# Kernel optimization log

Hardware: AMD Instinct MI355X
Metric: run time of the kernel (lower is better)

Reference implementation:

```python
import jax, jax.numpy as jnp
import numpy as np

N, IN_DIM, L, K, D = 131072, 128, 16, 8, 50
ENC_H, DEC_H, HEAD_H, DF = 64, 16, 64, 1.0


def setup_inputs() -> dict:
    key = jax.random.key(0)
    ks = jax.random.split(key, 20)
    s = lambda k, shape, fan: jax.random.normal(k, shape, jnp.float32) * (1.0 / np.sqrt(fan))
    return {
        "x": jax.random.normal(ks[0], (N, IN_DIM), jnp.float32),
        # encoder: in -> 64 -> 64 -> L
        "We1": s(ks[1], (IN_DIM, ENC_H), IN_DIM), "be1": jnp.zeros((ENC_H,), jnp.float32),
        "We2": s(ks[2], (ENC_H, ENC_H), ENC_H),   "be2": jnp.zeros((ENC_H,), jnp.float32),
        "We3": s(ks[3], (ENC_H, L), ENC_H),       "be3": jnp.zeros((L,), jnp.float32),
        # decoder: L -> 16 -> in
        "Wd1": s(ks[4], (L, DEC_H), L),           "bd1": jnp.zeros((DEC_H,), jnp.float32),
        "Wd2": s(ks[5], (DEC_H, IN_DIM), DEC_H),  "bd2": jnp.zeros((IN_DIM,), jnp.float32),
        # K per-cluster survival heads: (L+in) -> 64 -> num_durations
        "Wh1": s(ks[6], (K, L + IN_DIM, HEAD_H), L + IN_DIM), "bh1": jnp.zeros((K, HEAD_H), jnp.float32),
        "Wh2": s(ks[7], (K, HEAD_H, D), HEAD_H),              "bh2": jnp.zeros((K, D), jnp.float32),
        # cluster centers buffer
        "centers": jax.random.normal(ks[8], (K, L), jnp.float32) * 0.05,
    }


def _student_t_sim(z, centers, df):
    # z: [N, L], centers: [K, L] -> q: [N, K]
    dist2 = jnp.sum((z[:, None, :] - centers[None, :, :]) ** 2, axis=-1)
    logits = -0.5 * (df + 1.0) * jnp.log1p(dist2 / df)
    return jax.nn.softmax(logits, axis=1)


def reference(x, We1, be1, We2, be2, We3, be3, Wd1, bd1, Wd2, bd2,
              Wh1, bh1, Wh2, bh2, centers):
    relu = jax.nn.relu
    # encoder (eval mode: dropout off, non-variational)
    e = relu(x @ We1 + be1)
    e = relu(e @ We2 + be2)
    z = e @ We3 + be3                      # [N, L]
    q = _student_t_sim(z, centers, DF)     # [N, K]
    h = jnp.concatenate([z, x], axis=1)    # [N, L+in]
    # cluster-argmax routing to per-cluster heads: compute all K, select winner
    cluster_idx = jnp.argmax(q, axis=1)    # [N]
    h1 = relu(jnp.einsum("nf,kfh->nkh", h, Wh1) + bh1[None])   # [N, K, H]
    lg = jnp.einsum("nkh,khd->nkd", h1, Wh2) + bh2[None]       # [N, K, D]
    surv_logits = jnp.take_along_axis(lg, cluster_idx[:, None, None], axis=1)[:, 0]  # [N, D]
    # decoder + reconstruction loss per sample
    d = relu(z @ Wd1 + bd1)
    x_hat = d @ Wd2 + bd2                  # [N, in]
    rec_ps = jnp.mean((x_hat - x) ** 2, axis=1)
    kld = jnp.zeros((x.shape[0],), x.dtype)
    return z, q, surv_logits, x_hat, rec_ps, kld
```

## Files before the change

kernel.cpp:

```cpp
#include <hip/hip_runtime.h>

#define NS 131072
#define KC 8
typedef unsigned long long u64;

#define LD4(P) (*reinterpret_cast<const float4*>(&sm[(P)]))
#define ST4(P) (*reinterpret_cast<float4*>(&sm[(P)]))
#define GL4(P) (*reinterpret_cast<const float4*>(&(P)))

#define FMA4(ACCR, AV, B) do { \
  ACCR[0]=fmaf((AV),(B).x,ACCR[0]); ACCR[1]=fmaf((AV),(B).y,ACCR[1]); \
  ACCR[2]=fmaf((AV),(B).z,ACCR[2]); ACCR[3]=fmaf((AV),(B).w,ACCR[3]); } while(0)

#define K4(ACC, ABASE, ASTR, AK, BBASE, BSTR, JOFF, BK) do { \
  const float4 b0=LD4((BBASE)+((BK)*4+0)*(BSTR)+(JOFF)); \
  const float4 b1=LD4((BBASE)+((BK)*4+1)*(BSTR)+(JOFF)); \
  const float4 b2=LD4((BBASE)+((BK)*4+2)*(BSTR)+(JOFF)); \
  const float4 b3=LD4((BBASE)+((BK)*4+3)*(BSTR)+(JOFF)); \
  _Pragma("unroll") \
  for (int m_ = 0; m_ < 8; ++m_) { \
    const float4 av = LD4((ABASE)+(st+8*m_)*(ASTR)+(AK)*4); \
    FMA4(ACC[m_], av.x, b0); FMA4(ACC[m_], av.y, b1); \
    FMA4(ACC[m_], av.z, b2); FMA4(ACC[m_], av.w, b3); } \
} while(0)

#define INIT84(ACC, BPTR, OFF) do { \
  const float4 u_ = *reinterpret_cast<const float4*>(&(BPTR)[(OFF)]); \
  _Pragma("unroll") for (int m_=0;m_<8;++m_){ \
    ACC[m_][0]=u_.x; ACC[m_][1]=u_.y; ACC[m_][2]=u_.z; ACC[m_][3]=u_.w; } } while(0)

#define RELU84(ACC) do { _Pragma("unroll") for (int m_=0;m_<8;++m_) \
  { _Pragma("unroll") for (int j_=0;j_<4;++j_) ACC[m_][j_]=fmaxf(ACC[m_][j_],0.f); } } while(0)

#define WRITE_E(ACC) do { _Pragma("unroll") for (int m_=0;m_<8;++m_){ \
  ST4(EA + (st+8*m_)*68 + job) = \
    make_float4(ACC[m_][0],ACC[m_][1],ACC[m_][2],ACC[m_][3]); } } while(0)

#define STAGE_XB(B) do { \
  ST4((B) + xr0*20 + xcc)     = rx0; \
  ST4((B) + xr0*20 + xcc + 4) = rx1; } while(0)
#define STAGE_WB(B) do { \
  ST4((B) + wr*68 + wcc)     = rw0; \
  ST4((B) + wr*68 + wcc + 4) = rw1; } while(0)

#define XA   0
#define XB   1280
#define WA   2560
#define WB_  3648
#define EA   4736
#define ZD   4736
#define SMW  9088

__global__ __launch_bounds__(128, 2) void k_enc(
    const float* __restrict__ x,
    const float* __restrict__ We1, const float* __restrict__ be1,
    const float* __restrict__ We2, const float* __restrict__ be2,
    const float* __restrict__ We3, const float* __restrict__ be3,
    const float* __restrict__ Wd1, const float* __restrict__ bd1,
    const float* __restrict__ Wd2, const float* __restrict__ bd2,
    const float* __restrict__ centers,
    float* __restrict__ out_z, float* __restrict__ out_q,
    float* __restrict__ xhat, float* __restrict__ rec, float* __restrict__ kld,
    int* __restrict__ cidx, int* __restrict__ counts)
{
    __shared__ float sm[SMW];
    const int t  = threadIdx.x;
    const int ot = t & 15, st = t >> 4;
    const int job = ot * 4;
    const int s0 = blockIdx.x * 64;
    const int xr0 = t >> 1, xcc = (t & 1) * 8;
    const int wr  = t >> 3, wcc = (t & 7) * 8;

    {
        float acc1[8][4];
        INIT84(acc1, be1, job);
        ST4(XA + xr0*20 + xcc)     = GL4(x[(size_t)(s0+xr0)*128 + xcc]);
        ST4(XA + xr0*20 + xcc + 4) = GL4(x[(size_t)(s0+xr0)*128 + xcc + 4]);
        ST4(WA + wr*68 + wcc)      = GL4(We1[(size_t)wr*64 + wcc]);
        ST4(WA + wr*68 + wcc + 4)  = GL4(We1[(size_t)wr*64 + wcc + 4]);
        float4 rx0 = GL4(x[(size_t)(s0+xr0)*128 + 16 + xcc]);
        float4 rx1 = GL4(x[(size_t)(s0+xr0)*128 + 16 + xcc + 4]);
        float4 rw0 = GL4(We1[(size_t)(16 + wr)*64 + wcc]);
        float4 rw1 = GL4(We1[(size_t)(16 + wr)*64 + wcc + 4]);
        __syncthreads();
        #pragma unroll 1
        for (int c = 0; c < 8; ++c) {
            const int XC = (c & 1) ? XB : XA, WC = (c & 1) ? WB_ : WA;
            const int XN = (c & 1) ? XA : XB, WN = (c & 1) ? WA : WB_;
            #pragma unroll
            for (int kc = 0; kc < 4; ++kc) K4(acc1, XC, 20, kc, WC, 68, job, kc);
            if (c < 7) { STAGE_XB(XN); STAGE_WB(WN); }
            if (c < 6) {
                rx0 = GL4(x[(size_t)(s0+xr0)*128 + (c+2)*16 + xcc]);
                rx1 = GL4(x[(size_t)(s0+xr0)*128 + (c+2)*16 + xcc + 4]);
                rw0 = GL4(We1[(size_t)((c+2)*16 + wr)*64 + wcc]);
                rw1 = GL4(We1[(size_t)((c+2)*16 + wr)*64 + wcc + 4]);
            }
            if (c < 7) __syncthreads();
        }
        RELU84(acc1);
        WRITE_E(acc1);
    }

    {
        float acc2[8][4];
        INIT84(acc2, be2, job);
        ST4(WA + wr*68 + wcc)     = GL4(We2[(size_t)wr*64 + wcc]);
        ST4(WA + wr*68 + wcc + 4) = GL4(We2[(size_t)wr*64 + wcc + 4]);
        float4 rw0 = GL4(We2[(size_t)(16 + wr)*64 + wcc]);
        float4 rw1 = GL4(We2[(size_t)(16 + wr)*64 + wcc + 4]);
        __syncthreads();
        #pragma unroll 1
        for (int c = 0; c < 4; ++c) {
            const int WC = (c & 1) ? WB_ : WA, WN = (c & 1) ? WA : WB_;
            #pragma unroll
            for (int kc = 0; kc < 4; ++kc) K4(acc2, EA, 68, c*4 + kc, WC, 68, job, kc);
            if (c < 3) STAGE_WB(WN);
            if (c < 2) {
                rw0 = GL4(We2[(size_t)((c+2)*16 + wr)*64 + wcc]);
                rw1 = GL4(We2[(size_t)((c+2)*16 + wr)*64 + wcc + 4]);
            }
            if (c < 3) __syncthreads();
        }
        RELU84(acc2);
        WRITE_E(acc2);
    }

    ST4(XA + xr0*16 + xcc)     = GL4(We3[(size_t)xr0*16 + xcc]);
    ST4(XA + xr0*16 + xcc + 4) = GL4(We3[(size_t)xr0*16 + xcc + 4]);
    if (t < 32) {
        ST4(XB + (t>>1)*16 + (t&1)*8)     = GL4(Wd1[(t>>1)*16 + (t&1)*8]);
        ST4(XB + (t>>1)*16 + (t&1)*8 + 4) = GL4(Wd1[(t>>1)*16 + (t&1)*8 + 4]);
    }
    __syncthreads();

    float zac[8];
    {   const float b3v = be3[ot];
        #pragma unroll
        for (int m = 0; m < 8; ++m) zac[m] = b3v; }
    #pragma unroll 2
    for (int kc = 0; kc < 16; ++kc) {
        const float w0 = sm[XA + (kc*4+0)*16 + ot];
        const float w1 = sm[XA + (kc*4+1)*16 + ot];
        const float w2 = sm[XA + (kc*4+2)*16 + ot];
        const float w3 = sm[XA + (kc*4+3)*16 + ot];
        #pragma unroll
        for (int m = 0; m < 8; ++m) {
            const float4 av = LD4(EA + (st + 8*m)*68 + kc*4);
            float s = zac[m];
            s = fmaf(av.x, w0, s); s = fmaf(av.y, w1, s);
            s = fmaf(av.z, w2, s); s = fmaf(av.w, w3, s);
            zac[m] = s;
        }
    }
    #pragma unroll
    for (int m = 0; m < 8; ++m)
        out_z[(size_t)(s0 + st + 8*m)*16 + ot] = zac[m];
    __syncthreads();

    #pragma unroll
    for (int m = 0; m < 8; ++m) sm[ZD + (st + 8*m)*20 + ot] = zac[m];
    ST4(WA  + wr*68 + wcc)     = GL4(Wd2[(size_t)wr*128 + wcc]);
    ST4(WA  + wr*68 + wcc + 4) = GL4(Wd2[(size_t)wr*128 + wcc + 4]);
    ST4(WB_ + wr*68 + wcc)     = GL4(Wd2[(size_t)wr*128 + 64 + wcc]);
    ST4(WB_ + wr*68 + wcc + 4) = GL4(Wd2[(size_t)wr*128 + 64 + wcc + 4]);
    __syncthreads();

    if (t < 64) {
        const float4 z0 = LD4(ZD + t*20 + 0), z1 = LD4(ZD + t*20 + 4);
        const float4 z2 = LD4(ZD + t*20 + 8), z3 = LD4(ZD + t*20 + 12);
        const float zz[16] = {z0.x,z0.y,z0.z,z0.w, z1.x,z1.y,z1.z,z1.w,
                              z2.x,z2.y,z2.z,z2.w, z3.x,z3.y,z3.z,z3.w};
        float d2[KC];
        #pragma unroll
        for (int k = 0; k < KC; ++k) {
            float acc = 0.f;
            #pragma unroll
            for (int l = 0; l < 16; ++l) {
                const float dl = zz[l] - centers[k*16 + l];
                acc = fmaf(dl, dl, acc);
            }
            d2[k] = acc;
        }
        float lgt[KC], ex[KC];
        float mm = -1e30f;
        #pragma unroll
        for (int k = 0; k < KC; ++k) { lgt[k] = -log1pf(d2[k]); mm = fmaxf(mm, lgt[k]); }
        float ssum = 0.f;
        #pragma unroll
        for (int k = 0; k < KC; ++k) { ex[k] = expf(lgt[k] - mm); ssum += ex[k]; }
        const float inv = 1.f / ssum;
        float4* oq = reinterpret_cast<float4*>(&out_q[(size_t)(s0 + t)*8]);
        oq[0] = make_float4(ex[0]*inv, ex[1]*inv, ex[2]*inv, ex[3]*inv);
        oq[1] = make_float4(ex[4]*inv, ex[5]*inv, ex[6]*inv, ex[7]*inv);
        int ci = 0; float best = d2[0];
        #pragma unroll
        for (int k = 1; k < KC; ++k) if (d2[k] < best) { best = d2[k]; ci = k; }
        cidx[s0 + t] = ci;
        #pragma unroll
        for (int k = 0; k < KC; ++k) {
            const u64 mk = __ballot(ci == k);
            if (t == 0 && mk) atomicAdd(&counts[k], (int)__popcll(mk));
        }
        kld[s0 + t] = 0.f;
    }

    {
        float w[16];
        #pragma unroll
        for (int k = 0; k < 16; ++k) w[k] = sm[XB + k*16 + ot];
        const float bb = bd1[ot];
        float dac[8];
        #pragma unroll
        for (int m = 0; m < 8; ++m) {
            const int r = st + 8*m;
            float s = bb;
            #pragma unroll
            for (int kc = 0; kc < 4; ++kc) {
                const float4 av = LD4(ZD + r*20 + kc*4);
                s = fmaf(av.x, w[kc*4+0], s); s = fmaf(av.y, w[kc*4+1], s);
                s = fmaf(av.z, w[kc*4+2], s); s = fmaf(av.w, w[kc*4+3], s);
            }
            dac[m] = fmaxf(s, 0.f);
        }
        __syncthreads();
        #pragma unroll
        for (int m = 0; m < 8; ++m) sm[ZD + (st + 8*m)*20 + ot] = dac[m];
    }

    float rp[8] = {0.f,0.f,0.f,0.f,0.f,0.f,0.f,0.f};
    #pragma unroll
    for (int h = 0; h < 2; ++h) {
        const int WH = h ? WB_ : WA;
        float accx[8][4];
        INIT84(accx, bd2, h*64 + job);
        #pragma unroll
        for (int kc = 0; kc < 4; ++kc) K4(accx, ZD, 20, kc, WH, 68, job, kc);
        #pragma unroll
        for (int m = 0; m < 8; ++m) {
            const int r = st + 8*m;
            const float4 xa = GL4(x[(size_t)(s0+r)*128 + h*64 + job]);
            float df;
            df=accx[m][0]-xa.x; rp[m]=fmaf(df,df,rp[m]);
            df=accx[m][1]-xa.y; rp[m]=fmaf(df,df,rp[m]);
            df=accx[m][2]-xa.z; rp[m]=fmaf(df,df,rp[m]);
            df=accx[m][3]-xa.w; rp[m]=fmaf(df,df,rp[m]);
            *reinterpret_cast<float4*>(&xhat[(size_t)(s0+r)*128 + h*64 + job]) =
                make_float4(accx[m][0],accx[m][1],accx[m][2],accx[m][3]);
        }
    }
    #pragma unroll
    for (int m = 0; m < 8; ++m) {
        float v = rp[m];
        v += __shfl_xor(v, 1); v += __shfl_xor(v, 2);
        v += __shfl_xor(v, 4); v += __shfl_xor(v, 8);
        if (ot == 0) rec[s0 + st + 8*m] = v * (1.f/128.f);
    }
}

__global__ void k_scan(const int* __restrict__ counts,
                       int* __restrict__ bases, int* __restrict__ cursors)
{
    if (threadIdx.x == 0) {
        int acc = 0;
        for (int k = 0; k < KC; ++k) { bases[k] = acc; cursors[k] = acc; acc += counts[k]; }
    }
}

__global__ __launch_bounds__(256) void k_scatter(
    const int* __restrict__ cidx, int* __restrict__ cursors, int* __restrict__ seg)
{
    const int s = blockIdx.x * 256 + threadIdx.x;
    const int lane = threadIdx.x & 63;
    const int ci = cidx[s];
    #pragma unroll
    for (int k = 0; k < KC; ++k) {
        const u64 mk = __ballot(ci == k);
        if (ci == k) {
            const int leader = __ffsll(mk) - 1;
            int base = 0;
            if (lane == leader) base = atomicAdd(&cursors[k], (int)__popcll(mk));
            base = __shfl(base, leader, 64);
            seg[base + (int)__popcll(mk & (((u64)1 << lane) - 1))] = s;
        }
    }
}

__global__ __launch_bounds__(128, 2) void k_heads(
    const float* __restrict__ x, const float* __restrict__ zread,
    const float* __restrict__ Wh1, const float* __restrict__ bh1,
    const float* __restrict__ Wh2, const float* __restrict__ bh2,
    const int* __restrict__ counts, const int* __restrict__ bases,
    const int* __restrict__ seg,
    float* __restrict__ surv)
{
    __shared__ float sm[SMW];
    __shared__ int idxs[64];
    const int t  = threadIdx.x;
    const int ot = t & 15, st = t >> 4;
    const int job = ot * 4;
    const int xr0 = t >> 1, xcc = (t & 1) * 8;
    const int wr  = t >> 3, wcc = (t & 7) * 8;

    int kk = -1, chunk = 0, pref = 0;
    #pragma unroll
    for (int q = 0; q < KC; ++q) {
        const int ck = (counts[q] + 63) >> 6;
        if (kk < 0) {
            if ((int)blockIdx.x < pref + ck) { kk = q; chunk = (int)blockIdx.x - pref; }
            pref += ck;
        }
    }
    if (kk < 0) return;
    kk    = __builtin_amdgcn_readfirstlane(kk);
    chunk = __builtin_amdgcn_readfirstlane(chunk);
    const int cnt  = __builtin_amdgcn_readfirstlane(counts[kk]);
    const int base = __builtin_amdgcn_readfirstlane(bases[kk]);

    if (t < 64) {
        const int i = chunk*64 + t;
        idxs[t] = seg[base + ((i < cnt) ? i : (cnt - 1))];
    }
    __syncthreads();
    const int irow = idxs[xr0];

    {
        float acc1[8][4];
        INIT84(acc1, bh1, (size_t)kk*64 + job);
        ST4(XA + xr0*20 + xcc)     = GL4(zread[(size_t)irow*16 + xcc]);
        ST4(XA + xr0*20 + xcc + 4) = GL4(zread[(size_t)irow*16 + xcc + 4]);
        ST4(WA + wr*68 + wcc)      = GL4(Wh1[((size_t)kk*144 + wr)*64 + wcc]);
        ST4(WA + wr*68 + wcc + 4)  = GL4(Wh1[((size_t)kk*144 + wr)*64 + wcc + 4]);
        float4 rx0 = GL4(x[(size_t)irow*128 + xcc]);
        float4 rx1 = GL4(x[(size_t)irow*128 + xcc + 4]);
        float4 rw0 = GL4(Wh1[((size_t)kk*144 + 16 + wr)*64 + wcc]);
        float4 rw1 = GL4(Wh1[((size_t)kk*144 + 16 + wr)*64 + wcc + 4]);
        __syncthreads();
        #pragma unroll 1
        for (int c = 0; c < 9; ++c) {
            const int XC = (c & 1) ? XB : XA, WC = (c & 1) ? WB_ : WA;
            const int XN = (c & 1) ? XA : XB, WN = (c & 1) ? WA : WB_;
            #pragma unroll
            for (int kc = 0; kc < 4; ++kc) K4(acc1, XC, 20, kc, WC, 68, job, kc);
            if (c < 8) { STAGE_XB(XN); STAGE_WB(WN); }
            if (c < 7) {
                rx0 = GL4(x[(size_t)irow*128 + (c+1)*16 + xcc]);
                rx1 = GL4(x[(size_t)irow*128 + (c+1)*16 + xcc + 4]);
                rw0 = GL4(Wh1[((size_t)kk*144 + (c+2)*16 + wr)*64 + wcc]);
                rw1 = GL4(Wh1[((size_t)kk*144 + (c+2)*16 + wr)*64 + wcc + 4]);
            }
            if (c < 8) __syncthreads();
        }
        RELU84(acc1);
        WRITE_E(acc1);
    }
    __syncthreads();

    float acc2[8][4];
    {
        #pragma unroll
        for (int m = 0; m < 8; ++m) {
            acc2[m][0] = (job+0 < 50) ? bh2[(size_t)kk*50 + job+0] : 0.f;
            acc2[m][1] = (job+1 < 50) ? bh2[(size_t)kk*50 + job+1] : 0.f;
            acc2[m][2] = (job+2 < 50) ? bh2[(size_t)kk*50 + job+2] : 0.f;
            acc2[m][3] = (job+3 < 50) ? bh2[(size_t)kk*50 + job+3] : 0.f;
        }
    }
    #define LDWH2(RV0, RV1, CROW) do { \
        const size_t wrow_ = ((size_t)kk*64 + (CROW) + wr)*50; \
        RV0.x = (wcc+0 < 50) ? Wh2[wrow_ + wcc+0] : 0.f; \
        RV0.y = (wcc+1 < 50) ? Wh2[wrow_ + wcc+1] : 0.f; \
        RV0.z = (wcc+2 < 50) ? Wh2[wrow_ + wcc+2] : 0.f; \
        RV0.w = (wcc+3 < 50) ? Wh2[wrow_ + wcc+3] : 0.f; \
        RV1.x = (wcc+4 < 50) ? Wh2[wrow_ + wcc+4] : 0.f; \
        RV1.y = (wcc+5 < 50) ? Wh2[wrow_ + wcc+5] : 0.f; \
        RV1.z = (wcc+6 < 50) ? Wh2[wrow_ + wcc+6] : 0.f; \
        RV1.w = (wcc+7 < 50) ? Wh2[wrow_ + wcc+7] : 0.f; } while(0)
    {
        float4 rw0, rw1;
        LDWH2(rw0, rw1, 0);
        STAGE_WB(WA);
        LDWH2(rw0, rw1, 16);
        __syncthreads();
        #pragma unroll 1
        for (int c = 0; c < 4; ++c) {
            const int WC = (c & 1) ? WB_ : WA, WN = (c & 1) ? WA : WB_;
            #pragma unroll
            for (int kc = 0; kc < 4; ++kc) K4(acc2, EA, 68, c*4 + kc, WC, 68, job, kc);
            if (c < 3) STAGE_WB(WN);
            if (c < 2) LDWH2(rw0, rw1, (c+2)*16);
            if (c < 3) __syncthreads();
        }
    }
    #undef LDWH2

    #pragma unroll
    for (int m = 0; m < 8; ++m) {
        const int r = st + 8*m;
        if (chunk*64 + r < cnt) {
            float* so = &surv[(size_t)idxs[r]*50 + job];
            if (ot < 12) {
                *reinterpret_cast<float2*>(&so[0]) = make_float2(acc2[m][0], acc2[m][1]);
                *reinterpret_cast<float2*>(&so[2]) = make_float2(acc2[m][2], acc2[m][3]);
            } else if (ot == 12) {
                *reinterpret_cast<float2*>(&so[0]) = make_float2(acc2[m][0], acc2[m][1]);
            }
        }
    }
}

extern "C" void kernel_launch(void* const* d_in, const int* in_sizes, int n_in,
                              void* d_out, int out_size, void* d_ws, size_t ws_size,
                              hipStream_t stream)
{
    const float* x   = (const float*)d_in[0];
    const float* We1 = (const float*)d_in[1];
    const float* be1 = (const float*)d_in[2];
    const float* We2 = (const float*)d_in[3];
    const float* be2 = (const float*)d_in[4];
    const float* We3 = (const float*)d_in[5];
    const float* be3 = (const float*)d_in[6];
    const float* Wd1 = (const float*)d_in[7];
    const float* bd1 = (const float*)d_in[8];
    const float* Wd2 = (const float*)d_in[9];
    const float* bd2 = (const float*)d_in[10];
    const float* Wh1 = (const float*)d_in[11];
    const float* bh1 = (const float*)d_in[12];
    const float* Wh2 = (const float*)d_in[13];
    const float* bh2 = (const float*)d_in[14];
    const float* cen = (const float*)d_in[15];
    float* out = (float*)d_out;

    float* out_z  = out;
    float* out_q  = out + (size_t)NS * 16;
    float* out_sv = out + (size_t)NS * 24;
    float* out_xh = out + (size_t)NS * 74;
    float* out_rc = out + (size_t)NS * 202;
    float* out_kl = out + (size_t)NS * 203;

    int* cidx    = (int*)d_ws;
    int* counts  = cidx + NS;
    int* bases   = counts + KC;
    int* cursors = bases + KC;
    int* seg     = cursors + KC;

    hipMemsetAsync(counts, 0, KC * sizeof(int), stream);

    k_enc<<<dim3(NS / 64), dim3(128), 0, stream>>>(
        x, We1, be1, We2, be2, We3, be3, Wd1, bd1, Wd2, bd2, cen,
        out_z, out_q, out_xh, out_rc, out_kl, cidx, counts);

    k_scan<<<dim3(1), dim3(64), 0, stream>>>(counts, bases, cursors);

    k_scatter<<<dim3(NS / 256), dim3(256), 0, stream>>>(cidx, cursors, seg);

    k_heads<<<dim3(NS / 64 + KC), dim3(128), 0, stream>>>(
        x, out_z, Wh1, bh1, Wh2, bh2, counts, bases, seg, out_sv);
}
```

Measured before the change: 485.2 us.

## Stage GEMM tiles via async global-to-LDS loads in encoder and heads

Replaces register-staged double buffering of x, We1, We2, Wd2 and Wh1 tiles with __builtin_amdgcn_global_load_lds direct copies into unpadded LDS buffers. This removes the register round-trip and the VGPR pressure of holding prefetched tiles, and shrinks shared memory. In exchange, rows become unpadded with stride 16/64, which may add LDS bank conflicts. Correctness now depends on the barrier placement to order the async writes against reads.

```diff
diff --git a/kernel.cpp b/kernel.cpp
--- a/kernel.cpp
+++ b/kernel.cpp
@@ -8,15 +8,19 @@
 #define ST4(P) (*reinterpret_cast<float4*>(&sm[(P)]))
 #define GL4(P) (*reinterpret_cast<const float4*>(&(P)))
 
+#define ASYNC16(GP, LP) \
+  __builtin_amdgcn_global_load_lds((const __attribute__((address_space(1))) void*)(GP), \
+                                   (__attribute__((address_space(3))) void*)(LP), 16, 0, 0)
+
 #define FMA4(ACCR, AV, B) do { \
   ACCR[0]=fmaf((AV),(B).x,ACCR[0]); ACCR[1]=fmaf((AV),(B).y,ACCR[1]); \
   ACCR[2]=fmaf((AV),(B).z,ACCR[2]); ACCR[3]=fmaf((AV),(B).w,ACCR[3]); } while(0)
 
-#define K4(ACC, ABASE, ASTR, AK, BBASE, BSTR, JOFF, BK) do { \
-  const float4 b0=LD4((BBASE)+((BK)*4+0)*(BSTR)+(JOFF)); \
-  const float4 b1=LD4((BBASE)+((BK)*4+1)*(BSTR)+(JOFF)); \
-  const float4 b2=LD4((BBASE)+((BK)*4+2)*(BSTR)+(JOFF)); \
-  const float4 b3=LD4((BBASE)+((BK)*4+3)*(BSTR)+(JOFF)); \
+#define K4S(ACC, ABASE, ASTR, AK, BBASE, JOFF, BK) do { \
+  const float4 b0=LD4((BBASE)+((BK)*4+0)*64+(JOFF)); \
+  const float4 b1=LD4((BBASE)+((BK)*4+1)*64+(JOFF)); \
+  const float4 b2=LD4((BBASE)+((BK)*4+2)*64+(JOFF)); \
+  const float4 b3=LD4((BBASE)+((BK)*4+3)*64+(JOFF)); \
   _Pragma("unroll") \
   for (int m_ = 0; m_ < 8; ++m_) { \
     const float4 av = LD4((ABASE)+(st+8*m_)*(ASTR)+(AK)*4); \
@@ -36,20 +40,34 @@
   ST4(EA + (st+8*m_)*68 + job) = \
     make_float4(ACC[m_][0],ACC[m_][1],ACC[m_][2],ACC[m_][3]); } } while(0)
 
-#define STAGE_XB(B) do { \
-  ST4((B) + xr0*20 + xcc)     = rx0; \
-  ST4((B) + xr0*20 + xcc + 4) = rx1; } while(0)
-#define STAGE_WB(B) do { \
-  ST4((B) + wr*68 + wcc)     = rw0; \
-  ST4((B) + wr*68 + wcc + 4) = rw1; } while(0)
-
 #define XA   0
-#define XB   1280
-#define WA   2560
-#define WB_  3648
-#define EA   4736
-#define ZD   4736
-#define SMW  9088
+#define XB   1024
+#define WA   2048
+#define WB_  3072
+#define EA   4096
+#define ZD   4096
+#define SMW  8448
+
+#define ISSUE_XENC(BX, COL0) do { \
+  { const int r_ = (wv*2+0)*16 + (l>>2); \
+    ASYNC16(&x[(size_t)(s0+r_)*128 + (COL0) + (l&3)*4], &sm[(BX) + (wv*2+0)*256]); } \
+  { const int r_ = (wv*2+1)*16 + (l>>2); \
+    ASYNC16(&x[(size_t)(s0+r_)*128 + (COL0) + (l&3)*4], &sm[(BX) + (wv*2+1)*256]); } \
+} while(0)
+
+#define ISSUE_W16(BW, WPTR, ROW0) do { \
+  { const int r_ = (wv*2+0)*4 + (l>>4); \
+    ASYNC16(&(WPTR)[(size_t)((ROW0)+r_)*64 + (l&15)*4], &sm[(BW) + (wv*2+0)*256]); } \
+  { const int r_ = (wv*2+1)*4 + (l>>4); \
+    ASYNC16(&(WPTR)[(size_t)((ROW0)+r_)*64 + (l&15)*4], &sm[(BW) + (wv*2+1)*256]); } \
+} while(0)
+
+#define ISSUE_WD2(BW, HOFF) do { \
+  { const int r_ = (wv*2+0)*4 + (l>>4); \
+    ASYNC16(&Wd2[(size_t)r_*128 + (HOFF) + (l&15)*4], &sm[(BW) + (wv*2+0)*256]); } \
+  { const int r_ = (wv*2+1)*4 + (l>>4); \
+    ASYNC16(&Wd2[(size_t)r_*128 + (HOFF) + (l&15)*4], &sm[(BW) + (wv*2+1)*256]); } \
+} while(0)
 
 __global__ __launch_bounds__(128, 2) void k_enc(
     const float* __restrict__ x,
@@ -68,71 +86,49 @@
     const int ot = t & 15, st = t >> 4;
     const int job = ot * 4;
     const int s0 = blockIdx.x * 64;
-    const int xr0 = t >> 1, xcc = (t & 1) * 8;
-    const int wr  = t >> 3, wcc = (t & 7) * 8;
-
-    {
-        float acc1[8][4];
-        INIT84(acc1, be1, job);
-        ST4(XA + xr0*20 + xcc)     = GL4(x[(size_t)(s0+xr0)*128 + xcc]);
-        ST4(XA + xr0*20 + xcc + 4) = GL4(x[(size_t)(s0+xr0)*128 + xcc + 4]);
-        ST4(WA + wr*68 + wcc)      = GL4(We1[(size_t)wr*64 + wcc]);
-        ST4(WA + wr*68 + wcc + 4)  = GL4(We1[(size_t)wr*64 + wcc + 4]);
-        float4 rx0 = GL4(x[(size_t)(s0+xr0)*128 + 16 + xcc]);
-        float4 rx1 = GL4(x[(size_t)(s0+xr0)*128 + 16 + xcc + 4]);
-        float4 rw0 = GL4(We1[(size_t)(16 + wr)*64 + wcc]);
-        float4 rw1 = GL4(We1[(size_t)(16 + wr)*64 + wcc + 4]);
+    const int wv = t >> 6, l = t & 63;
+
+    float acc1[8][4];
+    INIT84(acc1, be1, job);
+    ISSUE_XENC(XA, 0);  ISSUE_W16(WA, We1, 0);
+    ISSUE_XENC(XB, 16); ISSUE_W16(WB_, We1, 16);
+    __syncthreads();
+    #pragma unroll 1
+    for (int c = 0; c < 8; ++c) {
+        const int XC = (c & 1) ? XB : XA, WC = (c & 1) ? WB_ : WA;
+        #pragma unroll
+        for (int kc = 0; kc < 4; ++kc) K4S(acc1, XC, 16, kc, WC, job, kc);
         __syncthreads();
-        #pragma unroll 1
-        for (int c = 0; c < 8; ++c) {
-            const int XC = (c & 1) ? XB : XA, WC = (c & 1) ? WB_ : WA;
-            const int XN = (c & 1) ? XA : XB, WN = (c & 1) ? WA : WB_;
-            #pragma unroll
-            for (int kc = 0; kc < 4; ++kc) K4(acc1, XC, 20, kc, WC, 68, job, kc);
-            if (c < 7) { STAGE_XB(XN); STAGE_WB(WN); }
-            if (c < 6) {
-                rx0 = GL4(x[(size_t)(s0+xr0)*128 + (c+2)*16 + xcc]);
-                rx1 = GL4(x[(size_t)(s0+xr0)*128 + (c+2)*16 + xcc + 4]);
-                rw0 = GL4(We1[(size_t)((c+2)*16 + wr)*64 + wcc]);
-                rw1 = GL4(We1[(size_t)((c+2)*16 + wr)*64 + wcc + 4]);
-            }
-            if (c < 7) __syncthreads();
-        }
-        RELU84(acc1);
-        WRITE_E(acc1);
-    }
+        if (c < 6) { ISSUE_XENC(XC, (c+2)*16); ISSUE_W16(WC, We1, (c+2)*16); }
+    }
+    RELU84(acc1);
+    WRITE_E(acc1);
 
     {
         float acc2[8][4];
         INIT84(acc2, be2, job);
-        ST4(WA + wr*68 + wcc)     = GL4(We2[(size_t)wr*64 + wcc]);
-        ST4(WA + wr*68 + wcc + 4) = GL4(We2[(size_t)wr*64 + wcc + 4]);
-        float4 rw0 = GL4(We2[(size_t)(16 + wr)*64 + wcc]);
-        float4 rw1 = GL4(We2[(size_t)(16 + wr)*64 + wcc + 4]);
+        ISSUE_W16(WA, We2, 0); ISSUE_W16(WB_, We2, 16);
         __syncthreads();
         #pragma unroll 1
         for (int c = 0; c < 4; ++c) {
-            const int WC = (c & 1) ? WB_ : WA, WN = (c & 1) ? WA : WB_;
+            const int WC = (c & 1) ? WB_ : WA;
             #pragma unroll
-            for (int kc = 0; kc < 4; ++kc) K4(acc2, EA, 68, c*4 + kc, WC, 68, job, kc);
-            if (c < 3) STAGE_WB(WN);
-            if (c < 2) {
-                rw0 = GL4(We2[(size_t)((c+2)*16 + wr)*64 + wcc]);
-                rw1 = GL4(We2[(size_t)((c+2)*16 + wr)*64 + wcc + 4]);
-            }
-            if (c < 3) __syncthreads();
+            for (int kc = 0; kc < 4; ++kc) K4S(acc2, EA, 68, c*4 + kc, WC, job, kc);
+            __syncthreads();
+            if (c < 2) ISSUE_W16(WC, We2, (c+2)*16);
         }
         RELU84(acc2);
         WRITE_E(acc2);
     }
 
-    ST4(XA + xr0*16 + xcc)     = GL4(We3[(size_t)xr0*16 + xcc]);
-    ST4(XA + xr0*16 + xcc + 4) = GL4(We3[(size_t)xr0*16 + xcc + 4]);
+    ST4(XA + (t>>1)*16 + (t&1)*8)     = GL4(We3[(size_t)(t>>1)*16 + (t&1)*8]);
+    ST4(XA + (t>>1)*16 + (t&1)*8 + 4) = GL4(We3[(size_t)(t>>1)*16 + (t&1)*8 + 4]);
     if (t < 32) {
         ST4(XB + (t>>1)*16 + (t&1)*8)     = GL4(Wd1[(t>>1)*16 + (t&1)*8]);
         ST4(XB + (t>>1)*16 + (t&1)*8 + 4) = GL4(Wd1[(t>>1)*16 + (t&1)*8 + 4]);
     }
     __syncthreads();
+    ISSUE_WD2(WA, 0); ISSUE_WD2(WB_, 64);
 
     float zac[8];
     {   const float b3v = be3[ot];
@@ -157,13 +153,8 @@
     for (int m = 0; m < 8; ++m)
         out_z[(size_t)(s0 + st + 8*m)*16 + ot] = zac[m];
     __syncthreads();
-
     #pragma unroll
     for (int m = 0; m < 8; ++m) sm[ZD + (st + 8*m)*20 + ot] = zac[m];
-    ST4(WA  + wr*68 + wcc)     = GL4(Wd2[(size_t)wr*128 + wcc]);
-    ST4(WA  + wr*68 + wcc + 4) = GL4(Wd2[(size_t)wr*128 + wcc + 4]);
-    ST4(WB_ + wr*68 + wcc)     = GL4(Wd2[(size_t)wr*128 + 64 + wcc]);
-    ST4(WB_ + wr*68 + wcc + 4) = GL4(Wd2[(size_t)wr*128 + 64 + wcc + 4]);
     __syncthreads();
 
     if (t < 64) {
@@ -176,8 +167,8 @@
         for (int k = 0; k < KC; ++k) {
             float acc = 0.f;
             #pragma unroll
-            for (int l = 0; l < 16; ++l) {
-                const float dl = zz[l] - centers[k*16 + l];
+            for (int q = 0; q < 16; ++q) {
+                const float dl = zz[q] - centers[k*16 + q];
                 acc = fmaf(dl, dl, acc);
             }
             d2[k] = acc;
@@ -235,7 +226,7 @@
         float accx[8][4];
         INIT84(accx, bd2, h*64 + job);
         #pragma unroll
-        for (int kc = 0; kc < 4; ++kc) K4(accx, ZD, 20, kc, WH, 68, job, kc);
+        for (int kc = 0; kc < 4; ++kc) K4S(accx, ZD, 20, kc, WH, job, kc);
         #pragma unroll
         for (int m = 0; m < 8; ++m) {
             const int r = st + 8*m;
@@ -285,6 +276,19 @@
         }
     }
 }
+
+#define ISSUE_ZH(BX) do { \
+  { const int r_ = (wv*2+0)*16 + (l>>2); \
+    ASYNC16(&zread[(size_t)idxs[r_]*16 + (l&3)*4], &sm[(BX) + (wv*2+0)*256]); } \
+  { const int r_ = (wv*2+1)*16 + (l>>2); \
+    ASYNC16(&zread[(size_t)idxs[r_]*16 + (l&3)*4], &sm[(BX) + (wv*2+1)*256]); } \
+} while(0)
+#define ISSUE_XH(BX, COL0) do { \
+  { const int r_ = (wv*2+0)*16 + (l>>2); \
+    ASYNC16(&x[(size_t)idxs[r_]*128 + (COL0) + (l&3)*4], &sm[(BX) + (wv*2+0)*256]); } \
+  { const int r_ = (wv*2+1)*16 + (l>>2); \
+    ASYNC16(&x[(size_t)idxs[r_]*128 + (COL0) + (l&3)*4], &sm[(BX) + (wv*2+1)*256]); } \
+} while(0)
 
 __global__ __launch_bounds__(128, 2) void k_heads(
     const float* __restrict__ x, const float* __restrict__ zread,
@@ -299,8 +303,8 @@
     const int t  = threadIdx.x;
     const int ot = t & 15, st = t >> 4;
     const int job = ot * 4;
-    const int xr0 = t >> 1, xcc = (t & 1) * 8;
-    const int wr  = t >> 3, wcc = (t & 7) * 8;
+    const int wv = t >> 6, l = t & 63;
+    const int wr = t >> 3, wcc = (t & 7) * 8;
 
     int kk = -1, chunk = 0, pref = 0;
     #pragma unroll
@@ -316,45 +320,29 @@
     chunk = __builtin_amdgcn_readfirstlane(chunk);
     const int cnt  = __builtin_amdgcn_readfirstlane(counts[kk]);
     const int base = __builtin_amdgcn_readfirstlane(bases[kk]);
+    const float* Wh1k = Wh1 + (size_t)kk * 144 * 64;
 
     if (t < 64) {
         const int i = chunk*64 + t;
         idxs[t] = seg[base + ((i < cnt) ? i : (cnt - 1))];
     }
     __syncthreads();
-    const int irow = idxs[xr0];
-
-    {
-        float acc1[8][4];
-        INIT84(acc1, bh1, (size_t)kk*64 + job);
-        ST4(XA + xr0*20 + xcc)     = GL4(zread[(size_t)irow*16 + xcc]);
-        ST4(XA + xr0*20 + xcc + 4) = GL4(zread[(size_t)irow*16 + xcc + 4]);
-        ST4(WA + wr*68 + wcc)      = GL4(Wh1[((size_t)kk*144 + wr)*64 + wcc]);
-        ST4(WA + wr*68 + wcc + 4)  = GL4(Wh1[((size_t)kk*144 + wr)*64 + wcc + 4]);
-        float4 rx0 = GL4(x[(size_t)irow*128 + xcc]);
-        float4 rx1 = GL4(x[(size_t)irow*128 + xcc + 4]);
-        float4 rw0 = GL4(Wh1[((size_t)kk*144 + 16 + wr)*64 + wcc]);
-        float4 rw1 = GL4(Wh1[((size_t)kk*144 + 16 + wr)*64 + wcc + 4]);
+
+    float acc1[8][4];
+    INIT84(acc1, bh1, (size_t)kk*64 + job);
+    ISSUE_ZH(XA);     ISSUE_W16(WA, Wh1k, 0);
+    ISSUE_XH(XB, 0);  ISSUE_W16(WB_, Wh1k, 16);
+    __syncthreads();
+    #pragma unroll 1
+    for (int c = 0; c < 9; ++c) {
+        const int XC = (c & 1) ? XB : XA, WC = (c & 1) ? WB_ : WA;
+        #pragma unroll
+        for (int kc = 0; kc < 4; ++kc) K4S(acc1, XC, 16, kc, WC, job, kc);
         __syncthreads();
-        #pragma unroll 1
-        for (int c = 0; c < 9; ++c) {
-            const int XC = (c & 1) ? XB : XA, WC = (c & 1) ? WB_ : WA;
-            const int XN = (c & 1) ? XA : XB, WN = (c & 1) ? WA : WB_;
-            #pragma unroll
-            for (int kc = 0; kc < 4; ++kc) K4(acc1, XC, 20, kc, WC, 68, job, kc);
-            if (c < 8) { STAGE_XB(XN); STAGE_WB(WN); }
-            if (c < 7) {
-                rx0 = GL4(x[(size_t)irow*128 + (c+1)*16 + xcc]);
-                rx1 = GL4(x[(size_t)irow*128 + (c+1)*16 + xcc + 4]);
-                rw0 = GL4(Wh1[((size_t)kk*144 + (c+2)*16 + wr)*64 + wcc]);
-                rw1 = GL4(Wh1[((size_t)kk*144 + (c+2)*16 + wr)*64 + wcc + 4]);
-            }
-            if (c < 8) __syncthreads();
-        }
-        RELU84(acc1);
-        WRITE_E(acc1);
-    }
-    __syncthreads();
+        if (c < 7) { ISSUE_XH(XC, (c+1)*16); ISSUE_W16(WC, Wh1k, (c+2)*16); }
+    }
+    RELU84(acc1);
+    WRITE_E(acc1);
 
     float acc2[8][4];
     {
@@ -379,15 +367,19 @@
     {
         float4 rw0, rw1;
         LDWH2(rw0, rw1, 0);
-        STAGE_WB(WA);
+        ST4(WA + wr*64 + wcc)     = rw0;
+        ST4(WA + wr*64 + wcc + 4) = rw1;
         LDWH2(rw0, rw1, 16);
         __syncthreads();
         #pragma unroll 1
         for (int c = 0; c < 4; ++c) {
             const int WC = (c & 1) ? WB_ : WA, WN = (c & 1) ? WA : WB_;
             #pragma unroll
-            for (int kc = 0; kc < 4; ++kc) K4(acc2, EA, 68, c*4 + kc, WC, 68, job, kc);
-            if (c < 3) STAGE_WB(WN);
+            for (int kc = 0; kc < 4; ++kc) K4S(acc2, EA, 68, c*4 + kc, WC, job, kc);
+            if (c < 3) {
+                ST4(WN + wr*64 + wcc)     = rw0;
+                ST4(WN + wr*64 + wcc + 4) = rw1;
+            }
             if (c < 2) LDWH2(rw0, rw1, (c+2)*16);
             if (c < 3) __syncthreads();
         }
```

After: 465.1 us. -4.1%, faster.
